# Performance work log

Hardware: AMD Instinct MI355X
Metric: run time of the kernel (lower is better)

Reference implementation:

```python
import jax, jax.numpy as jnp
import numpy as np

MOMENTUM = 0.5  # update_method='momentum'
EPS = 1e-12


def _l2norm(x):
    return x / jnp.sqrt(jnp.sum(x * x, axis=-1, keepdims=True) + EPS)


def setup_inputs() -> dict:
    key = jax.random.key(0)
    k1, k2, k3, k4, k5 = jax.random.split(key, 5)
    N, D, C, B = 200000, 256, 1000, 256
    inputs = _l2norm(jax.random.normal(k1, (B, D), dtype=jnp.float32))
    features = _l2norm(jax.random.normal(k2, (N, D), dtype=jnp.float32))
    cluster_mean = jax.random.normal(k3, (C, D), dtype=jnp.float32)
    labels = jax.random.randint(k4, (N,), 0, C)
    indexes = jax.random.randint(k5, (B,), 0, N)
    targets = labels[indexes]  # cluster id of each mini-batch sample
    return {
        "inputs": inputs,
        "features": features,
        "cluster_mean": cluster_mean,
        "indexes": indexes,
        "labels": labels,
        "targets": targets,
    }


def reference(inputs, features, cluster_mean, indexes, labels, targets):
    # HM.forward: logits against cluster centroids
    outputs = inputs @ cluster_mean.T  # [B, C]

    # HM.backward side effects (memory-bank maintenance), vectorized:
    # 1) momentum scatter update of the per-instance memory bank + L2 renorm
    new_rows = MOMENTUM * features[indexes] + (1.0 - MOMENTUM) * inputs
    new_rows = _l2norm(new_rows)
    feats = features.at[indexes].set(new_rows)

    # 2) naive cluster-mean recompute (get_mean_conv mean part) for touched clusters
    C = cluster_mean.shape[0]
    sums = jax.ops.segment_sum(feats, labels, num_segments=C)            # [C, D]
    cnts = jax.ops.segment_sum(jnp.ones((feats.shape[0],), feats.dtype), labels, num_segments=C)
    means = sums / jnp.maximum(cnts, 1.0)[:, None]
    touched = jnp.zeros((C,), dtype=bool).at[targets].set(True)
    new_cluster_mean = jnp.where(touched[:, None], means, cluster_mean)

    return outputs, feats, new_cluster_mean
```

## Files before the change

### kernel.cpp

```cpp
#include <hip/hip_runtime.h>

typedef float f32x4 __attribute__((ext_vector_type(4)));

#define B 256
#define D 256
#define N 200000
#define C 1000

#define K1_BLOCKS   2048
#define LOGITS_LO   0
#define NEWROWS_LO  256
#define TOUCH_BLK   512
#define HIST_LO     513
#define HIST_BLOCKS 64
#define COPY_LO     577
#define COPY_BLOCKS (K1_BLOCKS - COPY_LO)

#define WS_NEWROWS_OFF  0
#define WS_HIST_OFF     262144
#define WS_TOUCHED_OFF  266144
#define WS_NW_OFF       270144
#define WS_OFFS_OFF     270148
#define WS_FILLPOS_OFF  274148
#define WS_WROW_OFF     278148
#define WS_WLAB_OFF     279172
#define WS_WB_OFF       280196
#define WS_ROWLIST_OFF  281220
#define ZERO_WORDS      (2 * C + 1)

__global__ __launch_bounds__(256) void k0_zero(int* __restrict__ z) {
    int i = blockIdx.x * 256 + threadIdx.x;
    if (i < ZERO_WORDS) z[i] = 0;
}

__global__ __launch_bounds__(256) void k1_kernel(
    const float* __restrict__ inputs, const float* __restrict__ features,
    const float* __restrict__ cluster_mean, const int* __restrict__ indexes,
    const int* __restrict__ labels, const int* __restrict__ targets,
    float* __restrict__ out_logits, float* __restrict__ out_feats,
    float* __restrict__ new_rows, int* __restrict__ hist, int* __restrict__ touched)
{
    const int blk = blockIdx.x;
    const int t = threadIdx.x;

    if (blk >= COPY_LO) {
        const f32x4* src = (const f32x4*)features;
        f32x4*       dst = (f32x4*)out_feats;
        const int total4 = N * (D / 4);
        const int stride = COPY_BLOCKS * 256;
        int i = (blk - COPY_LO) * 256 + t;
        for (; i + 3 * stride < total4; i += 4 * stride) {
            f32x4 v0 = src[i];
            f32x4 v1 = src[i + stride];
            f32x4 v2 = src[i + 2 * stride];
            f32x4 v3 = src[i + 3 * stride];
            dst[i] = v0;
            dst[i + stride] = v1;
            dst[i + 2 * stride] = v2;
            dst[i + 3 * stride] = v3;
        }
        for (; i < total4; i += stride)
            dst[i] = src[i];
    } else if (blk < NEWROWS_LO) {
        __shared__ float sbuf[D];
        int b = blk - LOGITS_LO;
        sbuf[t] = inputs[b * D + t];
        __syncthreads();
        const f32x4* cmv = (const f32x4*)cluster_mean;
        for (int c = t; c < C; c += 256) {
            const f32x4* cm = cmv + (size_t)c * 64;
            float a0 = 0.f, a1 = 0.f, a2 = 0.f, a3 = 0.f;
            #pragma unroll 8
            for (int d4 = 0; d4 < 64; ++d4) {
                f32x4 v = cm[d4];
                const float* si = sbuf + d4 * 4;
                a0 += v.x * si[0];
                a1 += v.y * si[1];
                a2 += v.z * si[2];
                a3 += v.w * si[3];
            }
            out_logits[(size_t)b * C + c] = (a0 + a1) + (a2 + a3);
        }
    } else if (blk < TOUCH_BLK) {
        __shared__ float wpart[4];
        __shared__ float stot;
        int b = blk - NEWROWS_LO;
        int r = indexes[b];
        float x = 0.5f * features[(size_t)r * D + t] + 0.5f * inputs[b * D + t];
        float s = x * x;
        #pragma unroll
        for (int off = 32; off > 0; off >>= 1) s += __shfl_down(s, off);
        if ((t & 63) == 0) wpart[t >> 6] = s;
        __syncthreads();
        if (t == 0) stot = (wpart[0] + wpart[1]) + (wpart[2] + wpart[3]);
        __syncthreads();
        new_rows[b * D + t] = x / sqrtf(stot + 1e-12f);
    } else if (blk == TOUCH_BLK) {
        if (t < B) touched[targets[t]] = 1;
    } else {
        __shared__ int lh[C];
        for (int i = t; i < C; i += 256) lh[i] = 0;
        __syncthreads();
        const int stride = HIST_BLOCKS * 256;
        for (int i = (blk - HIST_LO) * 256 + t; i < N; i += stride)
            atomicAdd(&lh[labels[i]], 1);
        __syncthreads();
        for (int i = t; i < C; i += 256) {
            int v = lh[i];
            if (v) atomicAdd(&hist[i], v);
        }
    }
}

__global__ __launch_bounds__(256) void k2_kernel(
    const int* __restrict__ indexes, const int* __restrict__ labels,
    const float* __restrict__ new_rows, float* __restrict__ out_feats,
    const int* __restrict__ hist, int* __restrict__ offs, int* __restrict__ fillpos,
    int* __restrict__ nw, int* __restrict__ w_row, int* __restrict__ w_lab,
    int* __restrict__ w_b)
{
    const int blk = blockIdx.x;
    const int t = threadIdx.x;

    if (blk < 256) {
        __shared__ int sidx[B];
        __shared__ int lose;
        sidx[t] = indexes[t];
        if (t == 0) lose = 0;
        __syncthreads();
        int b = blk;
        int my = sidx[b];
        if (t > b && sidx[t] == my) lose = 1;
        __syncthreads();
        if (!lose) {
            out_feats[(size_t)my * D + t] = new_rows[b * D + t];
            if (t == 0) {
                int p = atomicAdd(nw, 1);
                w_row[p] = my;
                w_lab[p] = labels[my];
                w_b[p] = b;
            }
        }
    } else {
        __shared__ int swt[4];
        int base = t * 4;
        int h0 = (base + 0 < C) ? hist[base + 0] : 0;
        int h1 = (base + 1 < C) ? hist[base + 1] : 0;
        int h2 = (base + 2 < C) ? hist[base + 2] : 0;
        int h3 = (base + 3 < C) ? hist[base + 3] : 0;
        int tot = h0 + h1 + h2 + h3;
        int lane = t & 63;
        int scan = tot;
        #pragma unroll
        for (int off = 1; off < 64; off <<= 1) {
            int v = __shfl_up(scan, off);
            if (lane >= off) scan += v;
        }
        if (lane == 63) swt[t >> 6] = scan;
        __syncthreads();
        int wbase = 0;
        for (int i = 0; i < (t >> 6); ++i) wbase += swt[i];
        int excl = wbase + scan - tot;
        if (base + 0 < C) { offs[base + 0] = excl;                fillpos[base + 0] = excl; }
        if (base + 1 < C) { offs[base + 1] = excl + h0;           fillpos[base + 1] = excl + h0; }
        if (base + 2 < C) { offs[base + 2] = excl + h0 + h1;      fillpos[base + 2] = excl + h0 + h1; }
        if (base + 3 < C) { offs[base + 3] = excl + h0 + h1 + h2; fillpos[base + 3] = excl + h0 + h1 + h2; }
    }
}

__global__ __launch_bounds__(256) void fill_kernel(
    const int* __restrict__ labels, const int* __restrict__ touched,
    int* __restrict__ fillpos, int* __restrict__ rowlist)
{
    int i = blockIdx.x * 256 + threadIdx.x;
    if (i >= N) return;
    int lab = labels[i];
    if (touched[lab]) {
        int p = atomicAdd(&fillpos[lab], 1);
        rowlist[p] = i;
    }
}

__global__ __launch_bounds__(1024) void cm_kernel(
    const float* __restrict__ cluster_mean, const float* __restrict__ features,
    const float* __restrict__ new_rows, const int* __restrict__ touched,
    const int* __restrict__ hist, const int* __restrict__ offs,
    const int* __restrict__ rowlist, const int* __restrict__ nw,
    const int* __restrict__ w_row, const int* __restrict__ w_lab,
    const int* __restrict__ w_b, float* __restrict__ out_cm)
{
    const int c = blockIdx.x;
    const int d = threadIdx.x & 255;
    const int k = threadIdx.x >> 8;
    if (!touched[c]) {
        if (k == 0) out_cm[(size_t)c * D + d] = cluster_mean[(size_t)c * D + d];
        return;
    }
    __shared__ float red[3][256];
    const int cnt = hist[c];
    const int off = offs[c];
    float acc = 0.0f;
    #pragma unroll 4
    for (int j = k; j < cnt; j += 4)
        acc += features[(size_t)rowlist[off + j] * D + d];
    const int nwv = *nw;
    for (int j = k; j < nwv; j += 4) {
        if (w_lab[j] == c)
            acc += new_rows[w_b[j] * D + d] - features[(size_t)w_row[j] * D + d];
    }
    if (k > 0) red[k - 1][d] = acc;
    __syncthreads();
    if (k == 0) {
        float tot = acc + red[0][d] + red[1][d] + red[2][d];
        out_cm[(size_t)c * D + d] = tot / fmaxf((float)cnt, 1.0f);
    }
}

extern "C" void kernel_launch(void* const* d_in, const int* in_sizes, int n_in,
                              void* d_out, int out_size, void* d_ws, size_t ws_size,
                              hipStream_t stream) {
    const float* inputs       = (const float*)d_in[0];
    const float* features     = (const float*)d_in[1];
    const float* cluster_mean = (const float*)d_in[2];
    const int*   indexes      = (const int*)d_in[3];
    const int*   labels       = (const int*)d_in[4];
    const int*   targets      = (const int*)d_in[5];

    float* out_logits = (float*)d_out;
    float* out_feats  = out_logits + (size_t)B * C;
    float* out_cm     = out_feats + (size_t)N * D;

    char* ws = (char*)d_ws;
    float* new_rows = (float*)(ws + WS_NEWROWS_OFF);
    int*   hist     = (int*)(ws + WS_HIST_OFF);
    int*   touched  = (int*)(ws + WS_TOUCHED_OFF);
    int*   nw       = (int*)(ws + WS_NW_OFF);
    int*   offs     = (int*)(ws + WS_OFFS_OFF);
    int*   fillpos  = (int*)(ws + WS_FILLPOS_OFF);
    int*   w_row    = (int*)(ws + WS_WROW_OFF);
    int*   w_lab    = (int*)(ws + WS_WLAB_OFF);
    int*   w_b      = (int*)(ws + WS_WB_OFF);
    int*   rowlist  = (int*)(ws + WS_ROWLIST_OFF);

    k0_zero<<<(ZERO_WORDS + 255) / 256, 256, 0, stream>>>((int*)(ws + WS_HIST_OFF));
    k1_kernel<<<K1_BLOCKS, 256, 0, stream>>>(inputs, features, cluster_mean,
                                             indexes, labels, targets,
                                             out_logits, out_feats, new_rows,
                                             hist, touched);
    k2_kernel<<<257, 256, 0, stream>>>(indexes, labels, new_rows, out_feats,
                                       hist, offs, fillpos, nw, w_row, w_lab, w_b);
    fill_kernel<<<(N + 255) / 256, 256, 0, stream>>>(labels, touched, fillpos, rowlist);
    cm_kernel<<<C, 1024, 0, stream>>>(cluster_mean, features, new_rows, touched,
                                      hist, offs, rowlist, nw, w_row, w_lab, w_b,
                                      out_cm);
}
```

Measured before the change: 152.1 us.

## Split bulk feature copy into its own kernel and move dedup into setup kernel

```diff
diff --git a/kernel.cpp b/kernel.cpp
--- a/kernel.cpp
+++ b/kernel.cpp
@@ -7,14 +7,10 @@
 #define N 200000
 #define C 1000
 
-#define K1_BLOCKS   2048
-#define LOGITS_LO   0
-#define NEWROWS_LO  256
-#define TOUCH_BLK   512
-#define HIST_LO     513
+#define SIDE_BLOCKS 576
+#define HIST_LO     512
 #define HIST_BLOCKS 64
-#define COPY_LO     577
-#define COPY_BLOCKS (K1_BLOCKS - COPY_LO)
+#define COPY_GRID   2048
 
 #define WS_NEWROWS_OFF  0
 #define WS_HIST_OFF     262144
@@ -26,44 +22,53 @@
 #define WS_WLAB_OFF     279172
 #define WS_WB_OFF       280196
 #define WS_ROWLIST_OFF  281220
-#define ZERO_WORDS      (2 * C + 1)
-
-__global__ __launch_bounds__(256) void k0_zero(int* __restrict__ z) {
-    int i = blockIdx.x * 256 + threadIdx.x;
-    if (i < ZERO_WORDS) z[i] = 0;
-}
-
-__global__ __launch_bounds__(256) void k1_kernel(
+
+__global__ __launch_bounds__(256) void k0_kernel(
+    const int* __restrict__ indexes, const int* __restrict__ labels,
+    const int* __restrict__ targets, int* __restrict__ hist,
+    int* __restrict__ touched, int* __restrict__ nw, int* __restrict__ w_row,
+    int* __restrict__ w_lab, int* __restrict__ w_b)
+{
+    const int blk = blockIdx.x;
+    const int t = threadIdx.x;
+    if (blk == 0) {
+        __shared__ int sidx[B];
+        __shared__ int cnt;
+        for (int i = t; i < C; i += 256) touched[i] = 0;
+        sidx[t] = indexes[t];
+        if (t == 0) cnt = 0;
+        __syncthreads();
+        touched[targets[t]] = 1;
+        bool win = true;
+        for (int j = t + 1; j < B; ++j)
+            if (sidx[j] == sidx[t]) { win = false; break; }
+        if (win) {
+            int p = atomicAdd(&cnt, 1);
+            int r = sidx[t];
+            w_row[p] = r;
+            w_lab[p] = labels[r];
+            w_b[p] = t;
+        }
+        __syncthreads();
+        if (t == 0) *nw = cnt;
+    } else {
+        int i = (blk - 1) * 256 + t;
+        if (i < C) hist[i] = 0;
+    }
+}
+
+__global__ __launch_bounds__(256) void k_side(
     const float* __restrict__ inputs, const float* __restrict__ features,
     const float* __restrict__ cluster_mean, const int* __restrict__ indexes,
-    const int* __restrict__ labels, const int* __restrict__ targets,
-    float* __restrict__ out_logits, float* __restrict__ out_feats,
-    float* __restrict__ new_rows, int* __restrict__ hist, int* __restrict__ touched)
+    const int* __restrict__ labels, float* __restrict__ out_logits,
+    float* __restrict__ new_rows, int* __restrict__ hist)
 {
     const int blk = blockIdx.x;
     const int t = threadIdx.x;
 
-    if (blk >= COPY_LO) {
-        const f32x4* src = (const f32x4*)features;
-        f32x4*       dst = (f32x4*)out_feats;
-        const int total4 = N * (D / 4);
-        const int stride = COPY_BLOCKS * 256;
-        int i = (blk - COPY_LO) * 256 + t;
-        for (; i + 3 * stride < total4; i += 4 * stride) {
-            f32x4 v0 = src[i];
-            f32x4 v1 = src[i + stride];
-            f32x4 v2 = src[i + 2 * stride];
-            f32x4 v3 = src[i + 3 * stride];
-            dst[i] = v0;
-            dst[i + stride] = v1;
-            dst[i + 2 * stride] = v2;
-            dst[i + 3 * stride] = v3;
-        }
-        for (; i < total4; i += stride)
-            dst[i] = src[i];
-    } else if (blk < NEWROWS_LO) {
+    if (blk < 256) {
         __shared__ float sbuf[D];
-        int b = blk - LOGITS_LO;
+        int b = blk;
         sbuf[t] = inputs[b * D + t];
         __syncthreads();
         const f32x4* cmv = (const f32x4*)cluster_mean;
@@ -81,10 +86,10 @@
             }
             out_logits[(size_t)b * C + c] = (a0 + a1) + (a2 + a3);
         }
-    } else if (blk < TOUCH_BLK) {
+    } else if (blk < 512) {
         __shared__ float wpart[4];
         __shared__ float stot;
-        int b = blk - NEWROWS_LO;
+        int b = blk - 256;
         int r = indexes[b];
         float x = 0.5f * features[(size_t)r * D + t] + 0.5f * inputs[b * D + t];
         float s = x * x;
@@ -95,8 +100,6 @@
         if (t == 0) stot = (wpart[0] + wpart[1]) + (wpart[2] + wpart[3]);
         __syncthreads();
         new_rows[b * D + t] = x / sqrtf(stot + 1e-12f);
-    } else if (blk == TOUCH_BLK) {
-        if (t < B) touched[targets[t]] = 1;
     } else {
         __shared__ int lh[C];
         for (int i = t; i < C; i += 256) lh[i] = 0;
@@ -112,36 +115,25 @@
     }
 }
 
+__global__ __launch_bounds__(256, 8) void k_copy(
+    const f32x4* __restrict__ src, f32x4* __restrict__ dst)
+{
+    const int total4 = N * (D / 4);
+    const int stride = COPY_GRID * 256;
+    for (int i = blockIdx.x * 256 + threadIdx.x; i < total4; i += stride)
+        dst[i] = src[i];
+}
+
 __global__ __launch_bounds__(256) void k2_kernel(
-    const int* __restrict__ indexes, const int* __restrict__ labels,
     const float* __restrict__ new_rows, float* __restrict__ out_feats,
-    const int* __restrict__ hist, int* __restrict__ offs, int* __restrict__ fillpos,
-    int* __restrict__ nw, int* __restrict__ w_row, int* __restrict__ w_lab,
-    int* __restrict__ w_b)
+    const int* __restrict__ hist, int* __restrict__ offs,
+    int* __restrict__ fillpos, const int* __restrict__ nw,
+    const int* __restrict__ w_row, const int* __restrict__ w_b)
 {
     const int blk = blockIdx.x;
     const int t = threadIdx.x;
 
-    if (blk < 256) {
-        __shared__ int sidx[B];
-        __shared__ int lose;
-        sidx[t] = indexes[t];
-        if (t == 0) lose = 0;
-        __syncthreads();
-        int b = blk;
-        int my = sidx[b];
-        if (t > b && sidx[t] == my) lose = 1;
-        __syncthreads();
-        if (!lose) {
-            out_feats[(size_t)my * D + t] = new_rows[b * D + t];
-            if (t == 0) {
-                int p = atomicAdd(nw, 1);
-                w_row[p] = my;
-                w_lab[p] = labels[my];
-                w_b[p] = b;
-            }
-        }
-    } else {
+    if (blk == 0) {
         __shared__ int swt[4];
         int base = t * 4;
         int h0 = (base + 0 < C) ? hist[base + 0] : 0;
@@ -165,6 +157,10 @@
         if (base + 1 < C) { offs[base + 1] = excl + h0;           fillpos[base + 1] = excl + h0; }
         if (base + 2 < C) { offs[base + 2] = excl + h0 + h1;      fillpos[base + 2] = excl + h0 + h1; }
         if (base + 3 < C) { offs[base + 3] = excl + h0 + h1 + h2; fillpos[base + 3] = excl + h0 + h1 + h2; }
+    } else {
+        int q = blk - 1;
+        if (q < *nw)
+            out_feats[(size_t)w_row[q] * D + t] = new_rows[w_b[q] * D + t];
     }
 }
 
@@ -242,13 +238,14 @@
     int*   w_b      = (int*)(ws + WS_WB_OFF);
     int*   rowlist  = (int*)(ws + WS_ROWLIST_OFF);
 
-    k0_zero<<<(ZERO_WORDS + 255) / 256, 256, 0, stream>>>((int*)(ws + WS_HIST_OFF));
-    k1_kernel<<<K1_BLOCKS, 256, 0, stream>>>(inputs, features, cluster_mean,
-                                             indexes, labels, targets,
-                                             out_logits, out_feats, new_rows,
-                                             hist, touched);
-    k2_kernel<<<257, 256, 0, stream>>>(indexes, labels, new_rows, out_feats,
-                                       hist, offs, fillpos, nw, w_row, w_lab, w_b);
+    k0_kernel<<<5, 256, 0, stream>>>(indexes, labels, targets, hist, touched,
+                                     nw, w_row, w_lab, w_b);
+    k_side<<<SIDE_BLOCKS, 256, 0, stream>>>(inputs, features, cluster_mean,
+                                            indexes, labels, out_logits,
+                                            new_rows, hist);
+    k_copy<<<COPY_GRID, 256, 0, stream>>>((const f32x4*)features, (f32x4*)out_feats);
+    k2_kernel<<<257, 256, 0, stream>>>(new_rows, out_feats, hist, offs, fillpos,
+                                       nw, w_row, w_b);
     fill_kernel<<<(N + 255) / 256, 256, 0, stream>>>(labels, touched, fillpos, rowlist);
     cm_kernel<<<C, 1024, 0, stream>>>(cluster_mean, features, new_rows, touched,
                                       hist, offs, rowlist, nw, w_row, w_lab, w_b,
```

New measurement: 180.4 us. +18.6%, slower.
